# Performance work log

Hardware: AMD Instinct MI355X
Metric: run time of the kernel (lower is better)

The kernel has to match this reference:

```python
import jax, jax.numpy as jnp
import numpy as np

N = 50000   # num_semes / nodes
E = 800000  # edges
R = 8       # num_relations
D = 128     # embed_dim
H = 128     # rgcn_hidden_dim
EPS = 1e-5


def layer_norm(x, g, b):
    mu = jnp.mean(x, axis=-1, keepdims=True)
    var = jnp.mean(jnp.square(x - mu), axis=-1, keepdims=True)
    return (x - mu) * jax.lax.rsqrt(var + EPS) * g + b


def rgcn_conv(x, W, root, bias, edge_index, edge_type, num_relations):
    # PyG RGCNConv (default aggr='mean', root weight + bias):
    # out[i] = sum_r mean_{j in N_r(i)} x[j] @ W_r + x[i] @ root + bias
    src, dst = edge_index[0], edge_index[1]
    n = x.shape[0]
    seg = dst * num_relations + edge_type  # combined (node, relation) segment id
    msgs = x[src]  # [E, d_in]
    agg = jax.ops.segment_sum(msgs, seg, num_segments=n * num_relations)
    agg = agg.reshape(n, num_relations, -1)  # [N, R, d_in]
    cnt = jax.ops.segment_sum(jnp.ones((msgs.shape[0],), dtype=x.dtype), seg,
                              num_segments=n * num_relations)
    cnt = cnt.reshape(n, num_relations, 1)
    mean = agg / jnp.maximum(cnt, 1.0)  # zero where no edges of that relation
    out = jnp.einsum('nrd,rdo->no', mean, W) + x @ root + bias
    return out


def setup_inputs() -> dict:
    key = jax.random.key(0)
    ks = jax.random.split(key, 20)
    f32 = jnp.float32
    def glorot(k, shape):
        fan = shape[-2]
        return jax.random.normal(k, shape, dtype=f32) / np.float32(np.sqrt(fan))
    return {
        'node_ids':  jax.random.randint(ks[0], (N,), 0, N),
        'edge_index': jax.random.randint(ks[1], (2, E), 0, N),
        'edge_type': jax.random.randint(ks[2], (E,), 0, R),
        'emb':   jax.random.normal(ks[3], (N, D), dtype=f32) * 0.02,
        'W1':    glorot(ks[4], (R, D, H)),
        'root1': glorot(ks[5], (D, H)),
        'b1':    jnp.zeros((H,), f32),
        'g1':    jnp.ones((H,), f32),
        'be1':   jnp.zeros((H,), f32),
        'W2':    glorot(ks[6], (R, H, H)),
        'root2': glorot(ks[7], (H, H)),
        'b2':    jnp.zeros((H,), f32),
        'g2':    jnp.ones((H,), f32),
        'be2':   jnp.zeros((H,), f32),
        'W3':    glorot(ks[8], (R, H, D)),
        'root3': glorot(ks[9], (H, D)),
        'b3':    jnp.zeros((D,), f32),
    }


def reference(node_ids, edge_index, edge_type, emb,
              W1, root1, b1, g1, be1,
              W2, root2, b2, g2, be2,
              W3, root3, b3):
    x = emb[node_ids]                                  # sememe embedding lookup
    x = rgcn_conv(x, W1, root1, b1, edge_index, edge_type, R)
    x = jax.nn.relu(layer_norm(x, g1, be1))            # dropout: eval mode (identity)
    x = rgcn_conv(x, W2, root2, b2, edge_index, edge_type, R)
    x = jax.nn.relu(layer_norm(x, g2, be2))
    x = rgcn_conv(x, W3, root3, b3, edge_index, edge_type, R)
    return x
```

## Files before the change

### kernel.cpp

```cpp
#include <hip/hip_runtime.h>
#include <hip/hip_bf16.h>
#include <stdint.h>


#define N_NODES 50000
#define N_EDGES 800000
#define R_REL 8

typedef __bf16 bf16_8 __attribute__((ext_vector_type(8)));
typedef float floatx4 __attribute__((ext_vector_type(4)));
typedef unsigned short ushort8 __attribute__((ext_vector_type(8)));

static __device__ __forceinline__ float bf2f(unsigned short v) {
    unsigned u = ((unsigned)v) << 16;
    return __builtin_bit_cast(float, u);
}
static __device__ __forceinline__ unsigned short f2bf(float f) {
    unsigned u = __builtin_bit_cast(unsigned, f);
    u += 0x7FFFu + ((u >> 16) & 1u);
    return (unsigned short)(u >> 16);
}

__global__ void k_detect(const unsigned* __restrict__ g1, unsigned* __restrict__ flag) {
    if (threadIdx.x == 0 && blockIdx.x == 0)
        flag[0] = (g1[0] == 0x3F803F80u) ? 1u : 0u;
}


__global__ void k_zero(unsigned* __restrict__ p, int n_words) {
    int i = blockIdx.x * blockDim.x + threadIdx.x;
    int stride = gridDim.x * blockDim.x;
    for (; i < n_words; i += stride) p[i] = 0u;
}

__global__ void k_count(const int* __restrict__ ei, const int* __restrict__ et,
                        unsigned* __restrict__ cnt_nt, unsigned* __restrict__ deg) {
    int e = blockIdx.x * 256 + threadIdx.x;
    if (e >= N_EDGES) return;
    int dst = ei[N_EDGES + e];
    int t = et[e];
    atomicAdd(&cnt_nt[dst * R_REL + t], 1u);
    atomicAdd(&deg[dst], 1u);
}

#define SCAN_B 1024
#define SCAN_NB ((N_NODES + SCAN_B - 1) / SCAN_B)

__global__ void k_scan1(const unsigned* __restrict__ deg, unsigned* __restrict__ escan,
                        unsigned* __restrict__ bsum) {
    __shared__ unsigned wsum[16];
    int tid = threadIdx.x;
    int lane = tid & 63, wid = tid >> 6;
    int i = blockIdx.x * SCAN_B + tid;
    unsigned v = (i < N_NODES) ? deg[i] : 0u;
    unsigned incl = v;
#pragma unroll
    for (int d = 1; d < 64; d <<= 1) {
        unsigned t = __shfl_up(incl, d, 64);
        if (lane >= d) incl += t;
    }
    if (lane == 63) wsum[wid] = incl;
    __syncthreads();
    if (wid == 0 && lane < 16) {
        unsigned w = wsum[lane];
#pragma unroll
        for (int d = 1; d < 16; d <<= 1) {
            unsigned t = __shfl_up(w, d, 64);
            if (lane >= d) w += t;
        }
        wsum[lane] = w;
    }
    __syncthreads();
    unsigned woff = (wid == 0) ? 0u : wsum[wid - 1];
    if (i < N_NODES) escan[i] = woff + incl - v;
    if (tid == 0) bsum[blockIdx.x] = wsum[15];
}

__global__ void k_scan2(unsigned* __restrict__ bsum, unsigned* __restrict__ boff,
                        unsigned* __restrict__ offs) {
    int lane = threadIdx.x;
    unsigned b = (lane < SCAN_NB) ? bsum[lane] : 0u;
    unsigned incl = b;
#pragma unroll
    for (int d = 1; d < 64; d <<= 1) {
        unsigned t = __shfl_up(incl, d, 64);
        if (lane >= d) incl += t;
    }
    if (lane < SCAN_NB) boff[lane] = incl - b;
    if (lane == 63) offs[N_NODES] = incl;
}

__global__ void k_scan3(const unsigned* __restrict__ escan, const unsigned* __restrict__ boff,
                        unsigned* __restrict__ offs) {
    int i = blockIdx.x * SCAN_B + threadIdx.x;
    if (i < N_NODES) offs[i] = escan[i] + boff[blockIdx.x];
}

__global__ void k_fill(const int* __restrict__ ei, const int* __restrict__ et,
                       const unsigned* __restrict__ offs, unsigned* __restrict__ cursor,
                       unsigned* __restrict__ csr) {
    int e = blockIdx.x * 256 + threadIdx.x;
    if (e >= N_EDGES) return;
    int src = ei[e];
    int dst = ei[N_EDGES + e];
    int t = et[e];
    unsigned pos = offs[dst] + atomicAdd(&cursor[dst], 1u);
    csr[pos] = (unsigned)src | ((unsigned)t << 16);
}

__global__ void k_invcnt(const unsigned* __restrict__ cnt, float* __restrict__ inv) {
    int i = blockIdx.x * 256 + threadIdx.x;
    if (i >= N_NODES * R_REL) return;
    unsigned c = cnt[i];
    inv[i] = 1.0f / (float)(c ? c : 1u);
}

__global__ void k_transw(const unsigned* __restrict__ flag,
                         const void* __restrict__ W1, const void* __restrict__ r1,
                         const void* __restrict__ W2, const void* __restrict__ r2,
                         const void* __restrict__ W3, const void* __restrict__ r3,
                         unsigned short* __restrict__ WT) {
    int idx = blockIdx.x * 256 + threadIdx.x;
    if (idx >= 27 * 128 * 128) return;
    int is_bf = (int)flag[0];
    int m = idx >> 14;
    int r = idx & 16383;
    int o = r >> 7, d = r & 127;
    int l = m / 9, j = m % 9;
    const void* W = (l == 0) ? W1 : (l == 1) ? W2 : W3;
    const void* rt = (l == 0) ? r1 : (l == 1) ? r2 : r3;
    size_t eoff = (size_t)d * 128 + o;
    unsigned short v;
    if (j == 0) {
        v = is_bf ? ((const unsigned short*)rt)[eoff]
                  : f2bf(((const float*)rt)[eoff]);
    } else {
        size_t base = (size_t)(j - 1) * 16384;
        v = is_bf ? ((const unsigned short*)W)[base + eoff]
                  : f2bf(((const float*)W)[base + eoff]);
    }
    WT[idx] = v;
}

__global__ void k_gather(const unsigned* __restrict__ flag,
                         const int* __restrict__ ids, const void* __restrict__ emb,
                         unsigned short* __restrict__ x) {
    int c = blockIdx.x * 256 + threadIdx.x;
    if (c >= N_NODES * 32) return;
    int is_bf = (int)flag[0];
    int row = c >> 5, k = (c & 31) << 2;
    size_t s = (size_t)ids[row] * 128 + k;
    if (is_bf) {
        *(uint2*)&x[(size_t)row * 128 + k] = *(const uint2*)((const unsigned short*)emb + s);
    } else {
        const float4 f = *(const float4*)((const float*)emb + s);
        unsigned p0 = (unsigned)f2bf(f.x) | ((unsigned)f2bf(f.y) << 16);
        unsigned p1 = (unsigned)f2bf(f.z) | ((unsigned)f2bf(f.w) << 16);
        uint2 u; u.x = p0; u.y = p1;
        *(uint2*)&x[(size_t)row * 128 + k] = u;
    }
}

__global__ void k_cvtvec(const unsigned* __restrict__ flag,
                         const void* p0, const void* p1, const void* p2,
                         const void* p3, const void* p4, const void* p5,
                         const void* p6, float* __restrict__ vecs) {
    int v = blockIdx.x, i = threadIdx.x;
    const void* p = (v == 0) ? p0 : (v == 1) ? p1 : (v == 2) ? p2 :
                    (v == 3) ? p3 : (v == 4) ? p4 : (v == 5) ? p5 : p6;
    float f = flag[0] ? bf2f(((const unsigned short*)p)[i]) : ((const float*)p)[i];
    vecs[v * 128 + i] = f;
}


#define LDT 72

__global__ __launch_bounds__(256) void k_gemm(
    const unsigned short* __restrict__ X,
    const unsigned short* __restrict__ WT,
    const float* __restrict__ bias,
    unsigned short* __restrict__ y)
{
    __shared__ unsigned short As[128 * LDT];
    __shared__ unsigned short Bs[128 * LDT];
    int tid = threadIdx.x;
    int m0 = blockIdx.x * 128;
    int jb = blockIdx.y;
    int lane = tid & 63, wave = tid >> 6;
    int wm = (wave & 1) * 64, wn = (wave >> 1) * 64;
    int rr = lane & 15, qq = lane >> 4;

    floatx4 acc[4][4];
#pragma unroll
    for (int i = 0; i < 4; i++)
#pragma unroll
        for (int j = 0; j < 4; j++) acc[i][j] = (floatx4){0.f, 0.f, 0.f, 0.f};

    const unsigned short* Bsrc = WT + (size_t)jb * 16384;

#pragma unroll
    for (int ks = 0; ks < 2; ++ks) {
        int k0g = ks * 64;
#pragma unroll
        for (int i = 0; i < 4; ++i) {
            int c = tid + i * 256;
            int row = c >> 3;
            int kc = (c & 7) << 3;
            int grow = m0 + row;
            if (grow >= N_NODES) grow = N_NODES - 1;
            *(ushort8*)&As[row * LDT + kc] = *(const ushort8*)&X[(size_t)grow * 128 + k0g + kc];
            *(ushort8*)&Bs[row * LDT + kc] = *(const ushort8*)&Bsrc[row * 128 + k0g + kc];
        }
        __syncthreads();
#pragma unroll
        for (int kk = 0; kk < 2; ++kk) {
            int kb = kk * 32 + qq * 8;
            bf16_8 a[4], b[4];
#pragma unroll
            for (int i = 0; i < 4; i++) {
                a[i] = __builtin_bit_cast(bf16_8, *(const ushort8*)&As[(wm + i * 16 + rr) * LDT + kb]);
                b[i] = __builtin_bit_cast(bf16_8, *(const ushort8*)&Bs[(wn + i * 16 + rr) * LDT + kb]);
            }
#pragma unroll
            for (int i = 0; i < 4; i++)
#pragma unroll
                for (int j = 0; j < 4; j++)
                    acc[i][j] = __builtin_amdgcn_mfma_f32_16x16x32_bf16(a[i], b[j], acc[i][j], 0, 0, 0);
        }
        __syncthreads();
    }

#pragma unroll
    for (int i = 0; i < 4; i++) {
#pragma unroll
        for (int p = 0; p < 4; p++) {
            int row = m0 + wm + i * 16 + qq * 4 + p;
            if (row < N_NODES) {
#pragma unroll
                for (int j = 0; j < 4; j++) {
                    int col = wn + j * 16 + rr;
                    float v = acc[i][j][p];
                    if (jb == 0) v += bias[col];
                    y[(size_t)row * 1152 + (size_t)jb * 128 + col] = f2bf(v);
                }
            }
        }
    }
}


__global__ __launch_bounds__(256) void k_agg(
    const unsigned short* __restrict__ y,
    const unsigned* __restrict__ offs,
    const unsigned* __restrict__ csr,
    const float* __restrict__ invc,
    const float* __restrict__ g,
    const float* __restrict__ be,
    void* __restrict__ outp,
    int do_ln,
    const unsigned* __restrict__ flag)
{
    int n = blockIdx.x * 4 + (threadIdx.x >> 6);
    int lane = threadIdx.x & 63;
    int c0 = lane * 2;
    unsigned u0 = *(const unsigned*)&y[(size_t)n * 1152 + c0];
    float ax = bf2f((unsigned short)(u0 & 0xFFFFu));
    float ay = bf2f((unsigned short)(u0 >> 16));
    unsigned e0 = offs[n], e1 = offs[n + 1];
    float invw = (lane < R_REL) ? invc[n * R_REL + lane] : 0.f;

    for (unsigned base = e0; base < e1; base += 64) {
        int cnt = (int)min(64u, e1 - base);
        unsigned pk = (lane < cnt) ? csr[base + lane] : 0u;
        int j = 0;
        for (; j + 4 <= cnt; j += 4) {
            unsigned p0 = __shfl(pk, j, 64);
            unsigned p1 = __shfl(pk, j + 1, 64);
            unsigned p2 = __shfl(pk, j + 2, 64);
            unsigned p3 = __shfl(pk, j + 3, 64);
            unsigned v0 = *(const unsigned*)&y[(size_t)(p0 & 0xFFFFu) * 1152 + ((1u + (p0 >> 16)) << 7) + c0];
            unsigned v1 = *(const unsigned*)&y[(size_t)(p1 & 0xFFFFu) * 1152 + ((1u + (p1 >> 16)) << 7) + c0];
            unsigned v2 = *(const unsigned*)&y[(size_t)(p2 & 0xFFFFu) * 1152 + ((1u + (p2 >> 16)) << 7) + c0];
            unsigned v3 = *(const unsigned*)&y[(size_t)(p3 & 0xFFFFu) * 1152 + ((1u + (p3 >> 16)) << 7) + c0];
            float w0 = __shfl(invw, (int)(p0 >> 16), 64);
            float w1 = __shfl(invw, (int)(p1 >> 16), 64);
            float w2 = __shfl(invw, (int)(p2 >> 16), 64);
            float w3 = __shfl(invw, (int)(p3 >> 16), 64);
            ax += w0 * bf2f((unsigned short)(v0 & 0xFFFFu));
            ay += w0 * bf2f((unsigned short)(v0 >> 16));
            ax += w1 * bf2f((unsigned short)(v1 & 0xFFFFu));
            ay += w1 * bf2f((unsigned short)(v1 >> 16));
            ax += w2 * bf2f((unsigned short)(v2 & 0xFFFFu));
            ay += w2 * bf2f((unsigned short)(v2 >> 16));
            ax += w3 * bf2f((unsigned short)(v3 & 0xFFFFu));
            ay += w3 * bf2f((unsigned short)(v3 >> 16));
        }
        for (; j < cnt; ++j) {
            unsigned p = __shfl(pk, j, 64);
            unsigned v = *(const unsigned*)&y[(size_t)(p & 0xFFFFu) * 1152 + ((1u + (p >> 16)) << 7) + c0];
            float w = __shfl(invw, (int)(p >> 16), 64);
            ax += w * bf2f((unsigned short)(v & 0xFFFFu));
            ay += w * bf2f((unsigned short)(v >> 16));
        }
    }

    if (do_ln) {
        float s1 = ax + ay, s2 = ax * ax + ay * ay;
#pragma unroll
        for (int d = 1; d < 64; d <<= 1) {
            s1 += __shfl_xor(s1, d, 64);
            s2 += __shfl_xor(s2, d, 64);
        }
        float mu = s1 * (1.f / 128.f);
        float var = s2 * (1.f / 128.f) - mu * mu;
        float rs = rsqrtf(var + 1e-5f);
        float vx = (ax - mu) * rs * g[c0] + be[c0];
        float vy = (ay - mu) * rs * g[c0 + 1] + be[c0 + 1];
        vx = vx > 0.f ? vx : 0.f;
        vy = vy > 0.f ? vy : 0.f;
        *(unsigned*)&((unsigned short*)outp)[(size_t)n * 128 + c0] =
            (unsigned)f2bf(vx) | ((unsigned)f2bf(vy) << 16);
    } else {
        if (flag[0]) {
            *(unsigned*)&((unsigned short*)outp)[(size_t)n * 128 + c0] =
                (unsigned)f2bf(ax) | ((unsigned)f2bf(ay) << 16);
        } else {
            float2 o; o.x = ax; o.y = ay;
            *(float2*)&((float*)outp)[(size_t)n * 128 + c0] = o;
        }
    }
}


extern "C" void kernel_launch(void* const* d_in, const int* in_sizes, int n_in,
                              void* d_out, int out_size, void* d_ws, size_t ws_size,
                              hipStream_t stream) {
    const int* node_ids = (const int*)d_in[0];
    const int* ei = (const int*)d_in[1];
    const int* et = (const int*)d_in[2];
    const void* emb = d_in[3];
    const void* W1 = d_in[4];
    const void* r1 = d_in[5];
    const void* b1 = d_in[6];
    const void* g1 = d_in[7];
    const void* be1 = d_in[8];
    const void* W2 = d_in[9];
    const void* r2 = d_in[10];
    const void* b2 = d_in[11];
    const void* g2 = d_in[12];
    const void* be2 = d_in[13];
    const void* W3 = d_in[14];
    const void* r3 = d_in[15];
    const void* b3 = d_in[16];

    char* ws = (char*)d_ws;
    size_t off = 0;
    auto alloc = [&](size_t bytes) -> char* {
        char* p = ws + off;
        off = (off + bytes + 1023) & ~(size_t)1023;
        return p;
    };
    unsigned* cnt_nt = (unsigned*)alloc((size_t)N_NODES * R_REL * 4);
    unsigned* deg    = (unsigned*)alloc((size_t)N_NODES * 4);
    unsigned* cursor = (unsigned*)alloc((size_t)N_NODES * 4);
    size_t zero_end = off;
    unsigned* offs   = (unsigned*)alloc((size_t)(N_NODES + 1) * 4);
    unsigned* escan  = (unsigned*)alloc((size_t)N_NODES * 4);
    unsigned* bsum   = (unsigned*)alloc((size_t)SCAN_NB * 4);
    unsigned* boff   = (unsigned*)alloc((size_t)SCAN_NB * 4);
    unsigned* csr    = (unsigned*)alloc((size_t)N_EDGES * 4);
    float* invc      = (float*)alloc((size_t)N_NODES * R_REL * 4);
    unsigned short* WT = (unsigned short*)alloc((size_t)27 * 16384 * 2);
    float* vecs      = (float*)alloc((size_t)7 * 128 * 4);
    unsigned* flag   = (unsigned*)alloc(64);
    unsigned short* x  = (unsigned short*)alloc((size_t)N_NODES * 128 * 2);
    unsigned short* y  = (unsigned short*)alloc((size_t)N_NODES * 1152 * 2);
    (void)ws_size; (void)in_sizes; (void)n_in; (void)out_size;

    k_detect<<<1, 64, 0, stream>>>((const unsigned*)g1, flag);
    k_zero<<<512, 256, 0, stream>>>((unsigned*)ws, (int)(zero_end / 4));
    k_count<<<(N_EDGES + 255) / 256, 256, 0, stream>>>(ei, et, cnt_nt, deg);
    k_scan1<<<SCAN_NB, SCAN_B, 0, stream>>>(deg, escan, bsum);
    k_scan2<<<1, 64, 0, stream>>>(bsum, boff, offs);
    k_scan3<<<SCAN_NB, SCAN_B, 0, stream>>>(escan, boff, offs);
    k_fill<<<(N_EDGES + 255) / 256, 256, 0, stream>>>(ei, et, offs, cursor, csr);
    k_invcnt<<<(N_NODES * R_REL + 255) / 256, 256, 0, stream>>>(cnt_nt, invc);
    k_transw<<<(27 * 16384 + 255) / 256, 256, 0, stream>>>(flag, W1, r1, W2, r2, W3, r3, WT);
    k_cvtvec<<<7, 128, 0, stream>>>(flag, b1, g1, be1, b2, g2, be2, b3, vecs);
    k_gather<<<(N_NODES * 32 + 255) / 256, 256, 0, stream>>>(flag, node_ids, emb, x);

    dim3 ggrid((N_NODES + 127) / 128, 9);

    k_gemm<<<ggrid, 256, 0, stream>>>(x, WT + (size_t)0 * 9 * 16384, vecs + 0 * 128, y);
    k_agg<<<N_NODES / 4, 256, 0, stream>>>(y, offs, csr, invc, vecs + 1 * 128, vecs + 2 * 128, x, 1, flag);
    k_gemm<<<ggrid, 256, 0, stream>>>(x, WT + (size_t)1 * 9 * 16384, vecs + 3 * 128, y);
    k_agg<<<N_NODES / 4, 256, 0, stream>>>(y, offs, csr, invc, vecs + 4 * 128, vecs + 5 * 128, x, 1, flag);
    k_gemm<<<ggrid, 256, 0, stream>>>(x, WT + (size_t)2 * 9 * 16384, vecs + 6 * 128, y);
    k_agg<<<N_NODES / 4, 256, 0, stream>>>(y, offs, csr, invc, vecs + 1 * 128, vecs + 2 * 128, d_out, 0, flag);
}
```

Baseline: 509.4 us.

## Aggregate per-relation means first, then run one fused K=1152 GEMM with LayerNorm

Each layer now averages neighbour features per (node, relation) directly from the 128-wide node features into a concatenated buffer. A single GEMM with K=1152 (root plus 8 relations) then writes the output, with bias, LayerNorm and ReLU fused into its epilogue. This replaces the old order of transforming first into a 1152-wide buffer and gathering from it. The random gathers now hit a small 12.8 MB feature array instead of a 115 MB transformed one, and the separate aggregation and LayerNorm pass goes away. The CSR is sorted by (node, relation) using per-edge ranks from the counting atomics, which removes the second atomic pass and the inverse-count kernel. In exchange there is an extra 100 MB intermediate write and read, and the GEMM runs with one block column of 128 rows, which may limit occupancy.

```diff
diff --git a/kernel.cpp b/kernel.cpp
--- a/kernel.cpp
+++ b/kernel.cpp
@@ -6,6 +6,7 @@
 #define N_NODES 50000
 #define N_EDGES 800000
 #define R_REL 8
+#define NSEG (N_NODES * R_REL)
 
 typedef __bf16 bf16_8 __attribute__((ext_vector_type(8)));
 typedef float floatx4 __attribute__((ext_vector_type(4)));
@@ -34,17 +35,16 @@
 }
 
 __global__ void k_count(const int* __restrict__ ei, const int* __restrict__ et,
-                        unsigned* __restrict__ cnt_nt, unsigned* __restrict__ deg) {
+                        unsigned* __restrict__ cnt_nt, unsigned* __restrict__ rank) {
     int e = blockIdx.x * 256 + threadIdx.x;
     if (e >= N_EDGES) return;
     int dst = ei[N_EDGES + e];
     int t = et[e];
-    atomicAdd(&cnt_nt[dst * R_REL + t], 1u);
-    atomicAdd(&deg[dst], 1u);
+    rank[e] = atomicAdd(&cnt_nt[dst * R_REL + t], 1u);
 }
 
 #define SCAN_B 1024
-#define SCAN_NB ((N_NODES + SCAN_B - 1) / SCAN_B)
+#define SCAN_NB ((NSEG + SCAN_B - 1) / SCAN_B)
 
 __global__ void k_scan1(const unsigned* __restrict__ deg, unsigned* __restrict__ escan,
                         unsigned* __restrict__ bsum) {
@@ -52,7 +52,7 @@
     int tid = threadIdx.x;
     int lane = tid & 63, wid = tid >> 6;
     int i = blockIdx.x * SCAN_B + tid;
-    unsigned v = (i < N_NODES) ? deg[i] : 0u;
+    unsigned v = (i < NSEG) ? deg[i] : 0u;
     unsigned incl = v;
 #pragma unroll
     for (int d = 1; d < 64; d <<= 1) {
@@ -72,47 +72,45 @@
     }
     __syncthreads();
     unsigned woff = (wid == 0) ? 0u : wsum[wid - 1];
-    if (i < N_NODES) escan[i] = woff + incl - v;
+    if (i < NSEG) escan[i] = woff + incl - v;
     if (tid == 0) bsum[blockIdx.x] = wsum[15];
 }
 
-__global__ void k_scan2(unsigned* __restrict__ bsum, unsigned* __restrict__ boff,
+__global__ void k_scan2(const unsigned* __restrict__ bsum, unsigned* __restrict__ boff,
                         unsigned* __restrict__ offs) {
-    int lane = threadIdx.x;
-    unsigned b = (lane < SCAN_NB) ? bsum[lane] : 0u;
+    __shared__ unsigned ws[8];
+    int tid = threadIdx.x;
+    int lane = tid & 63, w = tid >> 6;
+    unsigned b = (tid < SCAN_NB) ? bsum[tid] : 0u;
     unsigned incl = b;
 #pragma unroll
     for (int d = 1; d < 64; d <<= 1) {
         unsigned t = __shfl_up(incl, d, 64);
         if (lane >= d) incl += t;
     }
-    if (lane < SCAN_NB) boff[lane] = incl - b;
-    if (lane == 63) offs[N_NODES] = incl;
+    if (lane == 63) ws[w] = incl;
+    __syncthreads();
+    unsigned wpre = 0;
+    for (int i = 0; i < w; ++i) wpre += ws[i];
+    if (tid < SCAN_NB) boff[tid] = wpre + incl - b;
+    if (tid == 511) offs[NSEG] = wpre + incl;
 }
 
 __global__ void k_scan3(const unsigned* __restrict__ escan, const unsigned* __restrict__ boff,
                         unsigned* __restrict__ offs) {
     int i = blockIdx.x * SCAN_B + threadIdx.x;
-    if (i < N_NODES) offs[i] = escan[i] + boff[blockIdx.x];
+    if (i < NSEG) offs[i] = escan[i] + boff[blockIdx.x];
 }
 
 __global__ void k_fill(const int* __restrict__ ei, const int* __restrict__ et,
-                       const unsigned* __restrict__ offs, unsigned* __restrict__ cursor,
+                       const unsigned* __restrict__ offs, const unsigned* __restrict__ rank,
                        unsigned* __restrict__ csr) {
     int e = blockIdx.x * 256 + threadIdx.x;
     if (e >= N_EDGES) return;
     int src = ei[e];
     int dst = ei[N_EDGES + e];
     int t = et[e];
-    unsigned pos = offs[dst] + atomicAdd(&cursor[dst], 1u);
-    csr[pos] = (unsigned)src | ((unsigned)t << 16);
-}
-
-__global__ void k_invcnt(const unsigned* __restrict__ cnt, float* __restrict__ inv) {
-    int i = blockIdx.x * 256 + threadIdx.x;
-    if (i >= N_NODES * R_REL) return;
-    unsigned c = cnt[i];
-    inv[i] = 1.0f / (float)(c ? c : 1u);
+    csr[offs[dst * R_REL + t] + rank[e]] = (unsigned)src;
 }
 
 __global__ void k_transw(const unsigned* __restrict__ flag,
@@ -172,35 +170,93 @@
     vecs[v * 128 + i] = f;
 }
 
+__global__ __launch_bounds__(256) void k_aggmean(
+    const unsigned short* __restrict__ X,
+    const unsigned* __restrict__ offs,
+    const unsigned* __restrict__ csr,
+    unsigned short* __restrict__ xc)
+{
+    int n = blockIdx.x * 4 + (threadIdx.x >> 6);
+    int lane = threadIdx.x & 63;
+    int c0 = lane * 2;
+    unsigned ov = (lane < 9) ? offs[n * R_REL + lane] : 0u;
+    unsigned eb = __shfl(ov, 0, 64);
+    unsigned ee = __shfl(ov, 8, 64);
+    float sx[8], sy[8];
+#pragma unroll
+    for (int r = 0; r < 8; ++r) { sx[r] = 0.f; sy[r] = 0.f; }
+
+    for (unsigned base = eb; base < ee; base += 64) {
+        unsigned cnt = min(64u, ee - base);
+        unsigned pk = (lane < cnt) ? csr[base + lane] : 0u;
+        unsigned top = base + cnt;
+#pragma unroll
+        for (int r = 0; r < 8; ++r) {
+            unsigned lo = __shfl(ov, r, 64);
+            unsigned hi = __shfl(ov, r + 1, 64);
+            lo = lo > base ? lo : base;
+            hi = hi < top ? hi : top;
+            int j = (int)(lo - base);
+            int jend = (hi > lo) ? (int)(hi - base) : j;
+            for (; j + 2 <= jend; j += 2) {
+                unsigned p0 = __shfl(pk, j, 64);
+                unsigned p1 = __shfl(pk, j + 1, 64);
+                unsigned v0 = *(const unsigned*)&X[(size_t)p0 * 128 + c0];
+                unsigned v1 = *(const unsigned*)&X[(size_t)p1 * 128 + c0];
+                sx[r] += bf2f((unsigned short)(v0 & 0xFFFFu)) + bf2f((unsigned short)(v1 & 0xFFFFu));
+                sy[r] += bf2f((unsigned short)(v0 >> 16)) + bf2f((unsigned short)(v1 >> 16));
+            }
+            if (j < jend) {
+                unsigned p = __shfl(pk, j, 64);
+                unsigned v = *(const unsigned*)&X[(size_t)p * 128 + c0];
+                sx[r] += bf2f((unsigned short)(v & 0xFFFFu));
+                sy[r] += bf2f((unsigned short)(v >> 16));
+            }
+        }
+    }
+
+#pragma unroll
+    for (int r = 0; r < 8; ++r) {
+        unsigned lo = __shfl(ov, r, 64);
+        unsigned hi = __shfl(ov, r + 1, 64);
+        unsigned c = hi - lo;
+        float inv = c ? (1.f / (float)c) : 0.f;
+        unsigned out = (unsigned)f2bf(sx[r] * inv) | ((unsigned)f2bf(sy[r] * inv) << 16);
+        *(unsigned*)&xc[(size_t)n * 1024 + r * 128 + c0] = out;
+    }
+}
+
 
 #define LDT 72
 
 __global__ __launch_bounds__(256) void k_gemm(
     const unsigned short* __restrict__ X,
-    const unsigned short* __restrict__ WT,
+    const unsigned short* __restrict__ XC,
+    const unsigned short* __restrict__ WTL,
     const float* __restrict__ bias,
-    unsigned short* __restrict__ y)
+    const float* __restrict__ g,
+    const float* __restrict__ be,
+    void* __restrict__ outp,
+    int do_ln,
+    const unsigned* __restrict__ flag)
 {
     __shared__ unsigned short As[128 * LDT];
     __shared__ unsigned short Bs[128 * LDT];
     int tid = threadIdx.x;
     int m0 = blockIdx.x * 128;
-    int jb = blockIdx.y;
     int lane = tid & 63, wave = tid >> 6;
-    int wm = (wave & 1) * 64, wn = (wave >> 1) * 64;
+    int wm = wave * 32;
     int rr = lane & 15, qq = lane >> 4;
 
-    floatx4 acc[4][4];
-#pragma unroll
-    for (int i = 0; i < 4; i++)
-#pragma unroll
-        for (int j = 0; j < 4; j++) acc[i][j] = (floatx4){0.f, 0.f, 0.f, 0.f};
-
-    const unsigned short* Bsrc = WT + (size_t)jb * 16384;
-
-#pragma unroll
-    for (int ks = 0; ks < 2; ++ks) {
-        int k0g = ks * 64;
+    floatx4 acc[2][8];
+#pragma unroll
+    for (int i = 0; i < 2; i++)
+#pragma unroll
+        for (int j = 0; j < 8; j++) acc[i][j] = (floatx4){0.f, 0.f, 0.f, 0.f};
+
+    for (int ks = 0; ks < 18; ++ks) {
+        int k0 = ks * 64;
+        const unsigned short* bsrc = WTL + (size_t)(k0 >> 7) * 16384 + (k0 & 127);
 #pragma unroll
         for (int i = 0; i < 4; ++i) {
             int c = tid + i * 256;
@@ -208,125 +264,91 @@
             int kc = (c & 7) << 3;
             int grow = m0 + row;
             if (grow >= N_NODES) grow = N_NODES - 1;
-            *(ushort8*)&As[row * LDT + kc] = *(const ushort8*)&X[(size_t)grow * 128 + k0g + kc];
-            *(ushort8*)&Bs[row * LDT + kc] = *(const ushort8*)&Bsrc[row * 128 + k0g + kc];
+            const unsigned short* asrc = (k0 < 128)
+                ? &X[(size_t)grow * 128 + k0 + kc]
+                : &XC[(size_t)grow * 1024 + (k0 - 128) + kc];
+            *(ushort8*)&As[row * LDT + kc] = *(const ushort8*)asrc;
+            *(ushort8*)&Bs[row * LDT + kc] = *(const ushort8*)&bsrc[row * 128 + kc];
         }
         __syncthreads();
 #pragma unroll
         for (int kk = 0; kk < 2; ++kk) {
             int kb = kk * 32 + qq * 8;
-            bf16_8 a[4], b[4];
-#pragma unroll
-            for (int i = 0; i < 4; i++) {
+            bf16_8 a[2], b[8];
+#pragma unroll
+            for (int i = 0; i < 2; i++)
                 a[i] = __builtin_bit_cast(bf16_8, *(const ushort8*)&As[(wm + i * 16 + rr) * LDT + kb]);
-                b[i] = __builtin_bit_cast(bf16_8, *(const ushort8*)&Bs[(wn + i * 16 + rr) * LDT + kb]);
-            }
-#pragma unroll
-            for (int i = 0; i < 4; i++)
-#pragma unroll
-                for (int j = 0; j < 4; j++)
+#pragma unroll
+            for (int j = 0; j < 8; j++)
+                b[j] = __builtin_bit_cast(bf16_8, *(const ushort8*)&Bs[(j * 16 + rr) * LDT + kb]);
+#pragma unroll
+            for (int i = 0; i < 2; i++)
+#pragma unroll
+                for (int j = 0; j < 8; j++)
                     acc[i][j] = __builtin_amdgcn_mfma_f32_16x16x32_bf16(a[i], b[j], acc[i][j], 0, 0, 0);
         }
         __syncthreads();
     }
 
-#pragma unroll
-    for (int i = 0; i < 4; i++) {
-#pragma unroll
-        for (int p = 0; p < 4; p++) {
-            int row = m0 + wm + i * 16 + qq * 4 + p;
-            if (row < N_NODES) {
-#pragma unroll
-                for (int j = 0; j < 4; j++) {
-                    int col = wn + j * 16 + rr;
-                    float v = acc[i][j][p];
-                    if (jb == 0) v += bias[col];
-                    y[(size_t)row * 1152 + (size_t)jb * 128 + col] = f2bf(v);
+    float bs_[8];
+#pragma unroll
+    for (int j = 0; j < 8; ++j) bs_[j] = bias[j * 16 + rr];
+
+    if (do_ln) {
+        float g_[8], be_[8];
+#pragma unroll
+        for (int j = 0; j < 8; ++j) { g_[j] = g[j * 16 + rr]; be_[j] = be[j * 16 + rr]; }
+        unsigned short* O = (unsigned short*)outp;
+#pragma unroll
+        for (int i = 0; i < 2; ++i) {
+#pragma unroll
+            for (int p = 0; p < 4; ++p) {
+                int row = m0 + wm + i * 16 + qq * 4 + p;
+                float v[8]; float s1 = 0.f, s2 = 0.f;
+#pragma unroll
+                for (int j = 0; j < 8; ++j) {
+                    v[j] = acc[i][j][p] + bs_[j];
+                    s1 += v[j]; s2 += v[j] * v[j];
+                }
+#pragma unroll
+                for (int d = 1; d < 16; d <<= 1) {
+                    s1 += __shfl_xor(s1, d, 64);
+                    s2 += __shfl_xor(s2, d, 64);
+                }
+                float mu = s1 * (1.f / 128.f);
+                float var = s2 * (1.f / 128.f) - mu * mu;
+                float rs = rsqrtf(var + 1e-5f);
+                if (row < N_NODES) {
+#pragma unroll
+                    for (int j = 0; j < 8; ++j) {
+                        float t = (v[j] - mu) * rs * g_[j] + be_[j];
+                        t = t > 0.f ? t : 0.f;
+                        O[(size_t)row * 128 + j * 16 + rr] = f2bf(t);
+                    }
                 }
             }
         }
-    }
-}
-
-
-__global__ __launch_bounds__(256) void k_agg(
-    const unsigned short* __restrict__ y,
-    const unsigned* __restrict__ offs,
-    const unsigned* __restrict__ csr,
-    const float* __restrict__ invc,
-    const float* __restrict__ g,
-    const float* __restrict__ be,
-    void* __restrict__ outp,
-    int do_ln,
-    const unsigned* __restrict__ flag)
-{
-    int n = blockIdx.x * 4 + (threadIdx.x >> 6);
-    int lane = threadIdx.x & 63;
-    int c0 = lane * 2;
-    unsigned u0 = *(const unsigned*)&y[(size_t)n * 1152 + c0];
-    float ax = bf2f((unsigned short)(u0 & 0xFFFFu));
-    float ay = bf2f((unsigned short)(u0 >> 16));
-    unsigned e0 = offs[n], e1 = offs[n + 1];
-    float invw = (lane < R_REL) ? invc[n * R_REL + lane] : 0.f;
-
-    for (unsigned base = e0; base < e1; base += 64) {
-        int cnt = (int)min(64u, e1 - base);
-        unsigned pk = (lane < cnt) ? csr[base + lane] : 0u;
-        int j = 0;
-        for (; j + 4 <= cnt; j += 4) {
-            unsigned p0 = __shfl(pk, j, 64);
-            unsigned p1 = __shfl(pk, j + 1, 64);
-            unsigned p2 = __shfl(pk, j + 2, 64);
-            unsigned p3 = __shfl(pk, j + 3, 64);
-            unsigned v0 = *(const unsigned*)&y[(size_t)(p0 & 0xFFFFu) * 1152 + ((1u + (p0 >> 16)) << 7) + c0];
-            unsigned v1 = *(const unsigned*)&y[(size_t)(p1 & 0xFFFFu) * 1152 + ((1u + (p1 >> 16)) << 7) + c0];
-            unsigned v2 = *(const unsigned*)&y[(size_t)(p2 & 0xFFFFu) * 1152 + ((1u + (p2 >> 16)) << 7) + c0];
-            unsigned v3 = *(const unsigned*)&y[(size_t)(p3 & 0xFFFFu) * 1152 + ((1u + (p3 >> 16)) << 7) + c0];
-            float w0 = __shfl(invw, (int)(p0 >> 16), 64);
-            float w1 = __shfl(invw, (int)(p1 >> 16), 64);
-            float w2 = __shfl(invw, (int)(p2 >> 16), 64);
-            float w3 = __shfl(invw, (int)(p3 >> 16), 64);
-            ax += w0 * bf2f((unsigned short)(v0 & 0xFFFFu));
-            ay += w0 * bf2f((unsigned short)(v0 >> 16));
-            ax += w1 * bf2f((unsigned short)(v1 & 0xFFFFu));
-            ay += w1 * bf2f((unsigned short)(v1 >> 16));
-            ax += w2 * bf2f((unsigned short)(v2 & 0xFFFFu));
-            ay += w2 * bf2f((unsigned short)(v2 >> 16));
-            ax += w3 * bf2f((unsigned short)(v3 & 0xFFFFu));
-            ay += w3 * bf2f((unsigned short)(v3 >> 16));
-        }
-        for (; j < cnt; ++j) {
-            unsigned p = __shfl(pk, j, 64);
-            unsigned v = *(const unsigned*)&y[(size_t)(p & 0xFFFFu) * 1152 + ((1u + (p >> 16)) << 7) + c0];
-            float w = __shfl(invw, (int)(p >> 16), 64);
-            ax += w * bf2f((unsigned short)(v & 0xFFFFu));
-            ay += w * bf2f((unsigned short)(v >> 16));
-        }
-    }
-
-    if (do_ln) {
-        float s1 = ax + ay, s2 = ax * ax + ay * ay;
-#pragma unroll
-        for (int d = 1; d < 64; d <<= 1) {
-            s1 += __shfl_xor(s1, d, 64);
-            s2 += __shfl_xor(s2, d, 64);
-        }
-        float mu = s1 * (1.f / 128.f);
-        float var = s2 * (1.f / 128.f) - mu * mu;
-        float rs = rsqrtf(var + 1e-5f);
-        float vx = (ax - mu) * rs * g[c0] + be[c0];
-        float vy = (ay - mu) * rs * g[c0 + 1] + be[c0 + 1];
-        vx = vx > 0.f ? vx : 0.f;
-        vy = vy > 0.f ? vy : 0.f;
-        *(unsigned*)&((unsigned short*)outp)[(size_t)n * 128 + c0] =
-            (unsigned)f2bf(vx) | ((unsigned)f2bf(vy) << 16);
     } else {
-        if (flag[0]) {
-            *(unsigned*)&((unsigned short*)outp)[(size_t)n * 128 + c0] =
-                (unsigned)f2bf(ax) | ((unsigned)f2bf(ay) << 16);
-        } else {
-            float2 o; o.x = ax; o.y = ay;
-            *(float2*)&((float*)outp)[(size_t)n * 128 + c0] = o;
+        int is_bf = (int)flag[0];
+#pragma unroll
+        for (int i = 0; i < 2; ++i) {
+#pragma unroll
+            for (int p = 0; p < 4; ++p) {
+                int row = m0 + wm + i * 16 + qq * 4 + p;
+                if (row < N_NODES) {
+                    if (is_bf) {
+                        unsigned short* O = (unsigned short*)outp;
+#pragma unroll
+                        for (int j = 0; j < 8; ++j)
+                            O[(size_t)row * 128 + j * 16 + rr] = f2bf(acc[i][j][p] + bs_[j]);
+                    } else {
+                        float* O = (float*)outp;
+#pragma unroll
+                        for (int j = 0; j < 8; ++j)
+                            O[(size_t)row * 128 + j * 16 + rr] = acc[i][j][p] + bs_[j];
+                    }
+                }
+            }
         }
     }
 }
@@ -360,41 +382,41 @@
         off = (off + bytes + 1023) & ~(size_t)1023;
         return p;
     };
-    unsigned* cnt_nt = (unsigned*)alloc((size_t)N_NODES * R_REL * 4);
-    unsigned* deg    = (unsigned*)alloc((size_t)N_NODES * 4);
-    unsigned* cursor = (unsigned*)alloc((size_t)N_NODES * 4);
+    unsigned* cnt_nt = (unsigned*)alloc((size_t)NSEG * 4);
     size_t zero_end = off;
-    unsigned* offs   = (unsigned*)alloc((size_t)(N_NODES + 1) * 4);
-    unsigned* escan  = (unsigned*)alloc((size_t)N_NODES * 4);
+    unsigned* rank   = (unsigned*)alloc((size_t)N_EDGES * 4);
+    unsigned* offs   = (unsigned*)alloc((size_t)(NSEG + 1) * 4);
+    unsigned* escan  = (unsigned*)alloc((size_t)NSEG * 4);
     unsigned* bsum   = (unsigned*)alloc((size_t)SCAN_NB * 4);
     unsigned* boff   = (unsigned*)alloc((size_t)SCAN_NB * 4);
     unsigned* csr    = (unsigned*)alloc((size_t)N_EDGES * 4);
-    float* invc      = (float*)alloc((size_t)N_NODES * R_REL * 4);
     unsigned short* WT = (unsigned short*)alloc((size_t)27 * 16384 * 2);
     float* vecs      = (float*)alloc((size_t)7 * 128 * 4);
     unsigned* flag   = (unsigned*)alloc(64);
-    unsigned short* x  = (unsigned short*)alloc((size_t)N_NODES * 128 * 2);
-    unsigned short* y  = (unsigned short*)alloc((size_t)N_NODES * 1152 * 2);
+    unsigned short* h  = (unsigned short*)alloc((size_t)N_NODES * 128 * 2);
+    unsigned short* xc = (unsigned short*)alloc((size_t)N_NODES * 1024 * 2);
     (void)ws_size; (void)in_sizes; (void)n_in; (void)out_size;
 
     k_detect<<<1, 64, 0, stream>>>((const unsigned*)g1, flag);
     k_zero<<<512, 256, 0, stream>>>((unsigned*)ws, (int)(zero_end / 4));
-    k_count<<<(N_EDGES + 255) / 256, 256, 0, stream>>>(ei, et, cnt_nt, deg);
-    k_scan1<<<SCAN_NB, SCAN_B, 0, stream>>>(deg, escan, bsum);
-    k_scan2<<<1, 64, 0, stream>>>(bsum, boff, offs);
+    k_count<<<(N_EDGES + 255) / 256, 256, 0, stream>>>(ei, et, cnt_nt, rank);
+    k_scan1<<<SCAN_NB, SCAN_B, 0, stream>>>(cnt_nt, escan, bsum);
+    k_scan2<<<1, 512, 0, stream>>>(bsum, boff, offs);
     k_scan3<<<SCAN_NB, SCAN_B, 0, stream>>>(escan, boff, offs);
-    k_fill<<<(N_EDGES + 255) / 256, 256, 0, stream>>>(ei, et, offs, cursor, csr);
-    k_invcnt<<<(N_NODES * R_REL + 255) / 256, 256, 0, stream>>>(cnt_nt, invc);
+    k_fill<<<(N_EDGES + 255) / 256, 256, 0, stream>>>(ei, et, offs, rank, csr);
     k_transw<<<(27 * 16384 + 255) / 256, 256, 0, stream>>>(flag, W1, r1, W2, r2, W3, r3, WT);
     k_cvtvec<<<7, 128, 0, stream>>>(flag, b1, g1, be1, b2, g2, be2, b3, vecs);
-    k_gather<<<(N_NODES * 32 + 255) / 256, 256, 0, stream>>>(flag, node_ids, emb, x);
-
-    dim3 ggrid((N_NODES + 127) / 128, 9);
-
-    k_gemm<<<ggrid, 256, 0, stream>>>(x, WT + (size_t)0 * 9 * 16384, vecs + 0 * 128, y);
-    k_agg<<<N_NODES / 4, 256, 0, stream>>>(y, offs, csr, invc, vecs + 1 * 128, vecs + 2 * 128, x, 1, flag);
-    k_gemm<<<ggrid, 256, 0, stream>>>(x, WT + (size_t)1 * 9 * 16384, vecs + 3 * 128, y);
-    k_agg<<<N_NODES / 4, 256, 0, stream>>>(y, offs, csr, invc, vecs + 4 * 128, vecs + 5 * 128, x, 1, flag);
-    k_gemm<<<ggrid, 256, 0, stream>>>(x, WT + (size_t)2 * 9 * 16384, vecs + 6 * 128, y);
-    k_agg<<<N_NODES / 4, 256, 0, stream>>>(y, offs, csr, invc, vecs + 1 * 128, vecs + 2 * 128, d_out, 0, flag);
-}
+    k_gather<<<(N_NODES * 32 + 255) / 256, 256, 0, stream>>>(flag, node_ids, emb, h);
+
+    dim3 ggrid((N_NODES + 127) / 128);
+
+    k_aggmean<<<N_NODES / 4, 256, 0, stream>>>(h, offs, csr, xc);
+    k_gemm<<<ggrid, 256, 0, stream>>>(h, xc, WT + (size_t)0 * 9 * 16384,
+                                      vecs + 0 * 128, vecs + 1 * 128, vecs + 2 * 128, h, 1, flag);
+    k_aggmean<<<N_NODES / 4, 256, 0, stream>>>(h, offs, csr, xc);
+    k_gemm<<<ggrid, 256, 0, stream>>>(h, xc, WT + (size_t)1 * 9 * 16384,
+                                      vecs + 3 * 128, vecs + 4 * 128, vecs + 5 * 128, h, 1, flag);
+    k_aggmean<<<N_NODES / 4, 256, 0, stream>>>(h, offs, csr, xc);
+    k_gemm<<<ggrid, 256, 0, stream>>>(h, xc, WT + (size_t)2 * 9 * 16384,
+                                      vecs + 6 * 128, vecs + 1 * 128, vecs + 2 * 128, d_out, 0, flag);
+}
```

After: 513.6 us. Within noise of the previous version (+0.8%).
